# Optimization experiments

Measured on AMD Instinct MI355X. Metric: run time of the kernel, lower is better.

## Reference

```python
import jax, jax.numpy as jnp
import numpy as np

B, N, E, T, DIN, H, G, ND, NT, L = 4, 10000, 320000, 16, 16, 64, 64, 16, 3, 7


def _mlp2(x, W1, b1, W2, b2):
    # Linear -> LeakyReLU -> (Dropout: eval identity) -> Linear -> LeakyReLU
    h = jax.nn.leaky_relu(x @ W1 + b1)
    return jax.nn.leaky_relu(h @ W2 + b2)


def _gcn_conv(x, src, dst, ew, nt, W1, b1, W2, b2):
    # x: [B,N,D], nt: [B,N,ND], ew: [*,E,1] broadcastable over batch
    x_in = _mlp2(jnp.concatenate([x, nt], axis=-1), W1, b1, W2, b2)  # [B,N,G]
    msgs = x_in[:, src, :] * ew                                      # gather + weight, [B,E,G]
    aggr = jnp.zeros(x_in.shape, x_in.dtype).at[:, dst, :].add(msgs) # scatter-add, [B,N,G]
    return x + aggr


def _gru(x, Wx, Wh, bx, bh):
    # PyTorch-style GRU over time axis. x: [B,N,T,DIN] -> hs: [T,B,N,H]
    xw = jnp.einsum('bntd,dh->tbnh', x, Wx) + bx  # precompute input projections [T,B,N,3H]
    h0 = jnp.zeros(x.shape[:2] + (Wh.shape[0],), x.dtype)

    def step(h, xw_t):
        hw = h @ Wh + bh
        xr, xz, xn = jnp.split(xw_t, 3, axis=-1)
        hr, hz, hn = jnp.split(hw, 3, axis=-1)
        r = jax.nn.sigmoid(xr + hr)
        z = jax.nn.sigmoid(xz + hz)
        n = jnp.tanh(xn + r * hn)
        h_new = (1 - z) * n + z * h
        return h_new, h_new

    _, hs = jax.lax.scan(step, h0, xw)
    return hs


def reference(input_day, edge_attr, gru_Wx, gru_Wh, gru_bx, gru_bh,
              rnn_fc_W, rnn_fc_b,
              e_emb, e_c0_W1, e_c0_b1, e_c0_W2, e_c0_b2,
              e_c1_W1, e_c1_b1, e_c1_W2, e_c1_b2,
              e_fm_W1, e_fm_b1, e_fm_W2, e_fm_b2,
              g_emb, g_c0_W1, g_c0_b1, g_c0_W2, g_c0_b2,
              g_c1_W1, g_c1_b1, g_c1_W2, g_c1_b2,
              gcn_fc_W, gcn_fc_b,
              edge_index, node_type_ids):
    src, dst = edge_index[0], edge_index[1]

    # KRNN encoder (GRU) + max over time + FC head
    hs = _gru(input_day, gru_Wx, gru_Wh, gru_bx, gru_bh)  # [T,B,N,H]
    rnn_out = hs.max(axis=0)                              # kr_out.max(dim=-2) -> [B,N,H]
    y_rnn = rnn_out @ rnn_fc_W + rnn_fc_b                 # [B,N,L]

    # EdgeNet: GCN stack on static edge_attr, then per-edge pair MLP -> gate
    nt_e = jnp.broadcast_to(e_emb[node_type_ids][None], (B, N, ND))
    ew0 = edge_attr.reshape(1, E, 1)
    x = rnn_out
    x = _gcn_conv(x, src, dst, ew0, nt_e, e_c0_W1, e_c0_b1, e_c0_W2, e_c0_b2)
    x = _gcn_conv(x, src, dst, ew0, nt_e, e_c1_W1, e_c1_b1, e_c1_W2, e_c1_b2)
    edge_x = jnp.concatenate([x[:, src, :], x[:, dst, :]], axis=-1)  # [B,E,2G]
    h = jax.nn.leaky_relu(edge_x @ e_fm_W1 + e_fm_b1)
    edge_gate = jax.nn.relu(h @ e_fm_W2 + e_fm_b2)                   # [B,E,1]

    # Main GCNNet with learned edge gates
    nt_g = jnp.broadcast_to(g_emb[node_type_ids][None], (B, N, ND))
    x = rnn_out
    x = _gcn_conv(x, src, dst, edge_gate, nt_g, g_c0_W1, g_c0_b1, g_c0_W2, g_c0_b2)
    x = _gcn_conv(x, src, dst, edge_gate, nt_g, g_c1_W1, g_c1_b1, g_c1_W2, g_c1_b2)
    y_gcn = x @ gcn_fc_W + gcn_fc_b                                  # [B,N,L]

    return y_rnn + y_gcn


def setup_inputs() -> dict:
    key = jax.random.key(0)
    ks = iter(jax.random.split(key, 48))

    def nrm(shape, s=0.1):
        return jax.random.normal(next(ks), shape, jnp.float32) * s

    inp = {}
    inp['input_day'] = jax.random.normal(next(ks), (B, N, T, DIN), jnp.float32)
    inp['edge_index'] = jax.random.randint(next(ks), (2, E), 0, N)
    inp['node_type_ids'] = jax.random.randint(next(ks), (N,), 0, NT)
    inp['edge_attr'] = jax.random.uniform(next(ks), (E,), jnp.float32)

    inp['gru_Wx'] = nrm((DIN, 3 * H))
    inp['gru_Wh'] = nrm((H, 3 * H))
    inp['gru_bx'] = jnp.zeros((3 * H,), jnp.float32)
    inp['gru_bh'] = jnp.zeros((3 * H,), jnp.float32)
    inp['rnn_fc_W'] = nrm((H, L))
    inp['rnn_fc_b'] = jnp.zeros((L,), jnp.float32)

    inp['e_emb'] = nrm((NT, ND))
    inp['g_emb'] = nrm((NT, ND))
    for pre, in_dim in (('e_c0', H + ND), ('e_c1', G + ND), ('g_c0', H + ND), ('g_c1', G + ND)):
        inp[pre + '_W1'] = nrm((in_dim, G))
        inp[pre + '_b1'] = jnp.zeros((G,), jnp.float32)
        inp[pre + '_W2'] = nrm((G, G))
        inp[pre + '_b2'] = jnp.zeros((G,), jnp.float32)

    inp['e_fm_W1'] = nrm((2 * G, G))
    inp['e_fm_b1'] = jnp.zeros((G,), jnp.float32)
    inp['e_fm_W2'] = nrm((G, 1))
    inp['e_fm_b2'] = jnp.zeros((1,), jnp.float32)

    inp['gcn_fc_W'] = nrm((G, L))
    inp['gcn_fc_b'] = jnp.zeros((L,), jnp.float32)
    return inp
```

## Files before the change

### kernel.cpp

```cpp
#include <hip/hip_runtime.h>
#include <hip/hip_bf16.h>

#define NB 4
#define NN 10000
#define NE 320000
#define BN 40000
#define NL 7

typedef float f32x4 __attribute__((ext_vector_type(4)));
typedef __bf16 bf16x8 __attribute__((ext_vector_type(8)));

__device__ __forceinline__ float bf2f(unsigned short u){
  unsigned x = ((unsigned)u) << 16;
  return __builtin_bit_cast(float, x);
}
__device__ __forceinline__ unsigned short f2bf(float f){
  unsigned u = __builtin_bit_cast(unsigned, f);
  u += 0x7fffu + ((u >> 16) & 1u);
  return (unsigned short)(u >> 16);
}
__device__ __forceinline__ __bf16 f2b(float f){
  return __builtin_bit_cast(__bf16, f2bf(f));
}
__device__ __forceinline__ bf16x8 zero8(){
  uint4 z = make_uint4(0u,0u,0u,0u);
  return __builtin_bit_cast(bf16x8, z);
}
__device__ __forceinline__ bf16x8 one8(){
  uint4 z = make_uint4(0x3f80u,0u,0u,0u);
  return __builtin_bit_cast(bf16x8, z);
}
__device__ __forceinline__ bf16x8 ld8bf(const unsigned short* p){
  uint4 u = *(const uint4*)p;
  return __builtin_bit_cast(bf16x8, u);
}
__device__ __forceinline__ unsigned pk2(float lo, float hi){
  unsigned r;
  asm("v_cvt_pk_bf16_f32 %0, %1, %2" : "=v"(r) : "v"(lo), "v"(hi));
  return r;
}
__device__ __forceinline__ bf16x8 ld8f(const float* p){
  float4 a = *(const float4*)p;
  float4 b = *(const float4*)(p+4);
  uint4 u = make_uint4(pk2(a.x,a.y), pk2(a.z,a.w), pk2(b.x,b.y), pk2(b.z,b.w));
  return __builtin_bit_cast(bf16x8, u);
}
__device__ __forceinline__ float frcp(float x){ return __builtin_amdgcn_rcpf(x); }
__device__ __forceinline__ float sigm(float x){ return frcp(1.f+__expf(-x)); }
__device__ __forceinline__ float tanh_(float x){ return 1.f - 2.f*frcp(__expf(2.f*x)+1.f); }
__device__ __forceinline__ float lrelu(float x){ return x > 0.f ? x : 0.01f*x; }

#define LDS_WAIT() asm volatile("s_waitcnt lgkmcnt(0)" ::: "memory")

__global__ __launch_bounds__(256, 2) void gru_kernel(
    const float* __restrict__ xd,
    const float* __restrict__ Wx,
    const float* __restrict__ Wh,
    const float* __restrict__ bx,
    const float* __restrict__ bh,
    float* __restrict__ rnn)
{
  __shared__ __attribute__((aligned(16))) unsigned short WhT[192][72];
  __shared__ __attribute__((aligned(16))) unsigned short WxT[192][40];
  __shared__ __attribute__((aligned(16))) unsigned short hb[4][16][76];
  int tid = threadIdx.x;
  int wave = tid >> 6, lane = tid & 63;
  int ln16 = lane & 15, quad = lane >> 4;

  for (int i = tid; i < 64*192; i += 256){
    int k = i / 192, n = i - k*192;
    WhT[n][k] = f2bf(Wh[i]);
  }
  for (int i = tid; i < 16*192; i += 256){
    int k = i / 192, n = i - k*192;
    WxT[n][k] = f2bf(Wx[i]);
    WxT[n][17+k] = 0;
  }
  if (tid < 192){
    float bias = (tid < 128) ? (bx[tid] + bh[tid]) : bx[tid];
    WxT[tid][16] = f2bf(bias);
  }
  for (int i = tid; i < 4*16*76; i += 256) ((unsigned short*)hb)[i] = 0;
  __syncthreads();

  int rowbase = blockIdx.x * 64 + wave * 16;

  bf16x8 whf[2][12];
  #pragma unroll
  for (int kt=0; kt<2; ++kt)
    #pragma unroll
    for (int nt=0; nt<12; ++nt)
      whf[kt][nt] = ld8bf(&WhT[nt*16 + ln16][kt*32 + quad*8]);

  f32x4 bhn2[4];
  #pragma unroll
  for (int j=0;j<4;++j)
    bhn2[j] = *(const f32x4*)(bh + 128 + j*16 + quad*4);

  f32x4 hprev[4], vmax[4];
  #pragma unroll
  for (int j=0;j<4;++j){
    hprev[j] = (f32x4){0.f,0.f,0.f,0.f};
    vmax[j]  = (f32x4){-1e30f,-1e30f,-1e30f,-1e30f};
  }

  const float* xrow = xd + (size_t)(rowbase + ln16) * 256;
  unsigned short* hrow = &hb[wave][ln16][0];

  bf16x8 axc;
  if (quad < 2) axc = ld8f(xrow + quad*8);
  else          axc = (quad == 2) ? one8() : zero8();

  for (int t = 0; t < 16; ++t){
    bf16x8 axn;
    if (quad < 2) axn = (t < 15) ? ld8f(xrow + (t+1)*16 + quad*8) : zero8();
    else          axn = (quad == 2) ? one8() : zero8();
    bf16x8 ah0 = ld8bf(hrow + quad*8);
    bf16x8 ah1 = ld8bf(hrow + 32 + quad*8);

    #pragma unroll
    for (int j=0;j<4;++j){
      bf16x8 xr = ld8bf(&WxT[j*16+ln16][quad*8]);
      bf16x8 xz = ld8bf(&WxT[(4+j)*16+ln16][quad*8]);
      bf16x8 xn = ld8bf(&WxT[(8+j)*16+ln16][quad*8]);
      f32x4 z4 = (f32x4){0.f,0.f,0.f,0.f};
      f32x4 ar = __builtin_amdgcn_mfma_f32_16x16x32_bf16(xr, axc, z4, 0,0,0);
      ar = __builtin_amdgcn_mfma_f32_16x16x32_bf16(whf[0][j], ah0, ar, 0,0,0);
      ar = __builtin_amdgcn_mfma_f32_16x16x32_bf16(whf[1][j], ah1, ar, 0,0,0);
      f32x4 az = __builtin_amdgcn_mfma_f32_16x16x32_bf16(xz, axc, z4, 0,0,0);
      az = __builtin_amdgcn_mfma_f32_16x16x32_bf16(whf[0][4+j], ah0, az, 0,0,0);
      az = __builtin_amdgcn_mfma_f32_16x16x32_bf16(whf[1][4+j], ah1, az, 0,0,0);
      f32x4 an = __builtin_amdgcn_mfma_f32_16x16x32_bf16(xn, axc, z4, 0,0,0);
      f32x4 ah = __builtin_amdgcn_mfma_f32_16x16x32_bf16(whf[0][8+j], ah0, bhn2[j], 0,0,0);
      ah = __builtin_amdgcn_mfma_f32_16x16x32_bf16(whf[1][8+j], ah1, ah, 0,0,0);
      f32x4 hv;
      #pragma unroll
      for (int i=0;i<4;++i){
        float Er = __expf(-ar[i]);
        float Ez = __expf(-az[i]);
        float pr = 1.f + Er, pz = 1.f + Ez;
        float D  = frcp(pr * pz);
        float r  = D * pz;
        float z  = D * pr;
        float nn = tanh_(an[i] + r * ah[i]);
        float h  = fmaf(z, hprev[j][i]-nn, nn);
        hprev[j][i] = h;
        vmax[j][i] = fmaxf(vmax[j][i], h);
        hv[i] = h;
      }
      *(uint2*)&hb[wave][ln16][j*16+quad*4] = make_uint2(pk2(hv[0],hv[1]), pk2(hv[2],hv[3]));
    }
    LDS_WAIT();
    axc = axn;
  }
  float* orow = rnn + (size_t)(rowbase + ln16)*64;
  #pragma unroll
  for (int j=0;j<4;++j)
    *(f32x4*)(orow + j*16 + quad*4) = vmax[j];
}

__global__ __launch_bounds__(256, 2) void mlp2_kernel(
    const float* __restrict__ x,
    const int* __restrict__ ntid,
    const float* __restrict__ emb,
    const float* __restrict__ W1,
    const float* __restrict__ b1,
    const float* __restrict__ W2,
    const float* __restrict__ b2,
    unsigned short* __restrict__ out)
{
  __shared__ __attribute__((aligned(16))) unsigned short W1T[64][96];
  __shared__ __attribute__((aligned(16))) unsigned short W2T[64][72];
  __shared__ __attribute__((aligned(16))) unsigned short hb[4][16][72];
  __shared__ float sb1[64], sb2[64];
  int tid = threadIdx.x;
  for (int i=tid;i<80*64;i+=256){ int k=i>>6, n=i&63; W1T[n][k]=f2bf(W1[i]); }
  for (int i=tid;i<64*16;i+=256){ int n=i>>4, k=80+(i&15); W1T[n][k]=0; }
  for (int i=tid;i<64*64;i+=256){ int k=i>>6, n=i&63; W2T[n][k]=f2bf(W2[i]); }
  if (tid<64){ sb1[tid]=b1[tid]; sb2[tid]=b2[tid]; }
  __syncthreads();

  int wave = tid>>6, lane = tid&63, ln16 = lane&15, quad = lane>>4;
  int row0 = blockIdx.x*64 + wave*16;
  int r_ = row0 + ln16;
  const float* xr = x + (size_t)r_*64;
  bf16x8 a0 = ld8f(xr + quad*8);
  bf16x8 a1 = ld8f(xr + 32 + quad*8);
  int id = ntid[r_ % NN];
  bf16x8 a2 = (quad<2) ? ld8f(emb + id*16 + quad*8) : zero8();

  f32x4 acc[4];
  #pragma unroll
  for (int nt=0;nt<4;++nt){
    float bb = sb1[nt*16+ln16];
    acc[nt] = (f32x4){bb,bb,bb,bb};
    acc[nt] = __builtin_amdgcn_mfma_f32_16x16x32_bf16(a0, ld8bf(&W1T[nt*16+ln16][quad*8]),    acc[nt], 0,0,0);
    acc[nt] = __builtin_amdgcn_mfma_f32_16x16x32_bf16(a1, ld8bf(&W1T[nt*16+ln16][32+quad*8]), acc[nt], 0,0,0);
    acc[nt] = __builtin_amdgcn_mfma_f32_16x16x32_bf16(a2, ld8bf(&W1T[nt*16+ln16][64+quad*8]), acc[nt], 0,0,0);
  }
  #pragma unroll
  for (int nt=0;nt<4;++nt)
    #pragma unroll
    for (int i=0;i<4;++i)
      hb[wave][quad*4+i][nt*16+ln16] = f2bf(lrelu(acc[nt][i]));
  LDS_WAIT();
  bf16x8 h0 = ld8bf(&hb[wave][ln16][quad*8]);
  bf16x8 h1 = ld8bf(&hb[wave][ln16][32+quad*8]);
  f32x4 acc2[4];
  #pragma unroll
  for (int nt=0;nt<4;++nt){
    float bb = sb2[nt*16+ln16];
    acc2[nt] = (f32x4){bb,bb,bb,bb};
    acc2[nt] = __builtin_amdgcn_mfma_f32_16x16x32_bf16(h0, ld8bf(&W2T[nt*16+ln16][quad*8]),    acc2[nt], 0,0,0);
    acc2[nt] = __builtin_amdgcn_mfma_f32_16x16x32_bf16(h1, ld8bf(&W2T[nt*16+ln16][32+quad*8]), acc2[nt], 0,0,0);
  }
  #pragma unroll
  for (int nt=0;nt<4;++nt)
    #pragma unroll
    for (int i=0;i<4;++i)
      out[(size_t)(row0+quad*4+i)*64 + nt*16+ln16] = f2bf(lrelu(acc2[nt][i]));
}

__global__ __launch_bounds__(256, 2) void uv_kernel(
    const float* __restrict__ x,
    const float* __restrict__ W1,
    unsigned short* __restrict__ uvp)
{
  __shared__ __attribute__((aligned(16))) unsigned short WT[128][72];
  int tid=threadIdx.x;
  for (int i=tid;i<64*64;i+=256){
    int k=i>>6, n=i&63;
    WT[n][k]    = f2bf(W1[i]);
    WT[64+n][k] = f2bf(W1[64*64 + i]);
  }
  __syncthreads();
  int wave=tid>>6, lane=tid&63, ln16=lane&15, quad=lane>>4;
  int row0 = blockIdx.x*64 + wave*16;
  const float* xr = x + (size_t)(row0+ln16)*64;
  bf16x8 a0 = ld8f(xr + quad*8);
  bf16x8 a1 = ld8f(xr + 32 + quad*8);
  f32x4 acc[8];
  #pragma unroll
  for (int nt=0;nt<8;++nt){
    acc[nt] = (f32x4){0.f,0.f,0.f,0.f};
    acc[nt] = __builtin_amdgcn_mfma_f32_16x16x32_bf16(a0, ld8bf(&WT[nt*16+ln16][quad*8]),    acc[nt], 0,0,0);
    acc[nt] = __builtin_amdgcn_mfma_f32_16x16x32_bf16(a1, ld8bf(&WT[nt*16+ln16][32+quad*8]), acc[nt], 0,0,0);
  }
  #pragma unroll
  for (int nt=0;nt<8;++nt)
    #pragma unroll
    for (int i=0;i<4;++i)
      uvp[(size_t)(row0+quad*4+i)*128 + nt*16+ln16] = f2bf(acc[nt][i]);
}

__global__ __launch_bounds__(256) void count_kernel(const int* __restrict__ ei, int* __restrict__ counts){
  int e = blockIdx.x*256+threadIdx.x;
  atomicAdd(&counts[ei[NE+e]], 1);
}
__global__ __launch_bounds__(1024) void scan_kernel(const int* __restrict__ counts,
                                                    int* __restrict__ rowptr, int* __restrict__ cursor){
  __shared__ int incl[10240];
  __shared__ int wsum[16];
  int tid=threadIdx.x, wave=tid>>6, lane=tid&63;
  int base = wave*640;
  int carry=0;
  #pragma unroll
  for (int c=0;c<10;++c){
    int i = base + c*64 + lane;
    int v = (i<NN)? counts[i] : 0;
    int s = v;
    #pragma unroll
    for (int off=1;off<64;off<<=1){
      int t_ = __shfl_up(s, off);
      if (lane>=off) s += t_;
    }
    s += carry;
    incl[base + c*64 + lane] = s;
    carry = __shfl(s, 63);
  }
  if (lane==63) wsum[wave]=carry;
  __syncthreads();
  if (wave==0){
    int w_ = (lane<16)? wsum[lane]:0;
    #pragma unroll
    for (int off=1;off<16;off<<=1){
      int t_ = __shfl_up(w_, off);
      if (lane>=off) w_ += t_;
    }
    if (lane<16) wsum[lane]=w_;
  }
  __syncthreads();
  int woff = (wave>0)? wsum[wave-1] : 0;
  #pragma unroll
  for (int c=0;c<10;++c){
    int i = base + c*64 + lane;
    if (i<NN){
      int excl = incl[i] + woff - counts[i];
      rowptr[i]=excl; cursor[i]=excl;
    }
  }
  if (tid==0) rowptr[NN]=wsum[15];
}
__global__ __launch_bounds__(256) void fill_kernel(const int* __restrict__ ei,
                                                   const float* __restrict__ ea,
                                                   int* __restrict__ cursor,
                                                   int* __restrict__ ssrc,
                                                   float* __restrict__ wcsr){
  int e = blockIdx.x*256+threadIdx.x;
  int d = ei[NE+e];
  int pos = atomicAdd(&cursor[d],1);
  ssrc[pos]=ei[e];
  wcsr[pos]=ea[e];
}

__global__ __launch_bounds__(256) void aggr_kernel(
    const float* x,
    const unsigned short* __restrict__ xin,
    const int* __restrict__ rowptr,
    const int* __restrict__ ssrc,
    const float* __restrict__ wp,
    int bstride,
    float* out)
{
  int tid=threadIdx.x;
  int wave=tid>>6, lane=tid&63;
  int sub=lane>>4, l=lane&15;
  int bid = blockIdx.x*4 + wave;
  int b = bid / NN, n = bid - b*NN;
  int p0 = rowptr[n], p1 = rowptr[n+1];
  const unsigned short* xb_ = xin + (size_t)b*NN*64;
  const float* wb = wp + (size_t)b*bstride;
  float a0=0.f, a1=0.f, a2=0.f, a3=0.f;
  #pragma unroll 4
  for (int p=p0+sub; p<p1; p+=4){
    int s = ssrc[p];
    float w = wb[p];
    uint2 m = *(const uint2*)(xb_ + (size_t)s*64 + l*4);
    a0 += bf2f((unsigned short)(m.x & 0xffffu)) * w;
    a1 += bf2f((unsigned short)(m.x >> 16)) * w;
    a2 += bf2f((unsigned short)(m.y & 0xffffu)) * w;
    a3 += bf2f((unsigned short)(m.y >> 16)) * w;
  }
  a0 += __shfl_xor(a0,16); a0 += __shfl_xor(a0,32);
  a1 += __shfl_xor(a1,16); a1 += __shfl_xor(a1,32);
  a2 += __shfl_xor(a2,16); a2 += __shfl_xor(a2,32);
  a3 += __shfl_xor(a3,16); a3 += __shfl_xor(a3,32);
  if (sub==0){
    float4 base = *(const float4*)(x + (size_t)bid*64 + l*4);
    float4 o; o.x=base.x+a0; o.y=base.y+a1; o.z=base.z+a2; o.w=base.w+a3;
    *(float4*)(out + (size_t)bid*64 + l*4) = o;
  }
}

__global__ __launch_bounds__(256) void aggr_final_kernel(
    const float* x,
    const unsigned short* __restrict__ xin,
    const int* __restrict__ rowptr,
    const int* __restrict__ ssrc,
    const float* __restrict__ wp,
    const float* __restrict__ rnn,
    const float* __restrict__ Wr, const float* __restrict__ br,
    const float* __restrict__ Wg, const float* __restrict__ bg,
    float* __restrict__ out)
{
  __shared__ float sWr[448], sWg[448], sb[7];
  int tid=threadIdx.x;
  for (int i=tid;i<448;i+=256){ sWr[i]=Wr[i]; sWg[i]=Wg[i]; }
  if (tid<7) sb[tid]=br[tid]+bg[tid];
  __syncthreads();
  int wave=tid>>6, lane=tid&63;
  int sub=lane>>4, l=lane&15;
  int bid = blockIdx.x*4 + wave;
  int b = bid / NN, n = bid - b*NN;
  int p0 = rowptr[n], p1 = rowptr[n+1];
  const unsigned short* xb_ = xin + (size_t)b*NN*64;
  const float* wb = wp + (size_t)b*NE;
  float a0=0.f, a1=0.f, a2=0.f, a3=0.f;
  #pragma unroll 4
  for (int p=p0+sub; p<p1; p+=4){
    int s = ssrc[p];
    float w = wb[p];
    uint2 m = *(const uint2*)(xb_ + (size_t)s*64 + l*4);
    a0 += bf2f((unsigned short)(m.x & 0xffffu)) * w;
    a1 += bf2f((unsigned short)(m.x >> 16)) * w;
    a2 += bf2f((unsigned short)(m.y & 0xffffu)) * w;
    a3 += bf2f((unsigned short)(m.y >> 16)) * w;
  }
  a0 += __shfl_xor(a0,16); a0 += __shfl_xor(a0,32);
  a1 += __shfl_xor(a1,16); a1 += __shfl_xor(a1,32);
  a2 += __shfl_xor(a2,16); a2 += __shfl_xor(a2,32);
  a3 += __shfl_xor(a3,16); a3 += __shfl_xor(a3,32);
  if (sub==0){
    float4 base = *(const float4*)(x + (size_t)bid*64 + l*4);
    float o0=base.x+a0, o1=base.y+a1, o2=base.z+a2, o3=base.w+a3;
    float4 rr = *(const float4*)(rnn + (size_t)bid*64 + l*4);
    float part[7];
    #pragma unroll
    for (int q=0;q<7;++q)
      part[q] = o0*sWg[(l*4+0)*7+q] + o1*sWg[(l*4+1)*7+q]
              + o2*sWg[(l*4+2)*7+q] + o3*sWg[(l*4+3)*7+q]
              + rr.x*sWr[(l*4+0)*7+q] + rr.y*sWr[(l*4+1)*7+q]
              + rr.z*sWr[(l*4+2)*7+q] + rr.w*sWr[(l*4+3)*7+q];
    #pragma unroll
    for (int q=0;q<7;++q){
      part[q] += __shfl_xor(part[q],1);
      part[q] += __shfl_xor(part[q],2);
      part[q] += __shfl_xor(part[q],4);
      part[q] += __shfl_xor(part[q],8);
    }
    if (l==0){
      #pragma unroll
      for (int q=0;q<7;++q) out[(size_t)bid*7+q] = part[q] + sb[q];
    }
  }
}

__global__ __launch_bounds__(256) void gate_kernel(
    const unsigned short* __restrict__ uvp,
    const int* __restrict__ rowptr,
    const int* __restrict__ ssrc,
    const float* __restrict__ b1,
    const float* __restrict__ W2,
    const float* __restrict__ b2,
    float* __restrict__ gate)
{
  int tid=threadIdx.x;
  int wave=tid>>6, lane=tid&63;
  int sub=lane>>4, l=lane&15;
  int bid = blockIdx.x*4 + wave;
  int b = bid / NN, n = bid - b*NN;
  int p0 = rowptr[n], p1 = rowptr[n+1];
  const unsigned short* ub = uvp + (size_t)b*NN*128;
  uint2 vu = *(const uint2*)(ub + (size_t)n*128 + 64 + l*4);
  float v0=bf2f((unsigned short)(vu.x&0xffffu)), v1=bf2f((unsigned short)(vu.x>>16));
  float v2=bf2f((unsigned short)(vu.y&0xffffu)), v3=bf2f((unsigned short)(vu.y>>16));
  float4 bb = *(const float4*)(b1 + l*4);
  float4 ww = *(const float4*)(W2 + l*4);
  float b2v = b2[0];
  float* gb = gate + (size_t)b*NE;
  #pragma unroll 4
  for (int p=p0+sub; p<p1; p+=4){
    int s = ssrc[p];
    uint2 uu = *(const uint2*)(ub + (size_t)s*128 + l*4);
    float h0 = lrelu(bf2f((unsigned short)(uu.x&0xffffu)) + v0 + bb.x);
    float h1 = lrelu(bf2f((unsigned short)(uu.x>>16))     + v1 + bb.y);
    float h2 = lrelu(bf2f((unsigned short)(uu.y&0xffffu)) + v2 + bb.z);
    float h3 = lrelu(bf2f((unsigned short)(uu.y>>16))     + v3 + bb.w);
    float part = h0*ww.x + h1*ww.y + h2*ww.z + h3*ww.w;
    part += __shfl_xor(part,1);
    part += __shfl_xor(part,2);
    part += __shfl_xor(part,4);
    part += __shfl_xor(part,8);
    if (l==0){
      float g = part + b2v;
      gb[p] = g>0.f ? g : 0.f;
    }
  }
}

extern "C" void kernel_launch(void* const* d_in, const int* in_sizes, int n_in,
                              void* d_out, int out_size, void* d_ws, size_t ws_size,
                              hipStream_t stream)
{
  (void)in_sizes; (void)n_in; (void)out_size; (void)ws_size;
  const float* input_day = (const float*)d_in[0];
  const int* ei    = (const int*)d_in[1];
  const int* ntid  = (const int*)d_in[2];
  const float* edge_attr = (const float*)d_in[3];
  const float* gWx = (const float*)d_in[4];
  const float* gWh = (const float*)d_in[5];
  const float* gbx = (const float*)d_in[6];
  const float* gbh = (const float*)d_in[7];
  const float* rW  = (const float*)d_in[8];
  const float* rb  = (const float*)d_in[9];
  const float* eemb= (const float*)d_in[10];
  const float* gemb= (const float*)d_in[11];
  const float* ec0W1=(const float*)d_in[12];
  const float* ec0b1=(const float*)d_in[13];
  const float* ec0W2=(const float*)d_in[14];
  const float* ec0b2=(const float*)d_in[15];
  const float* ec1W1=(const float*)d_in[16];
  const float* ec1b1=(const float*)d_in[17];
  const float* ec1W2=(const float*)d_in[18];
  const float* ec1b2=(const float*)d_in[19];
  const float* gc0W1=(const float*)d_in[20];
  const float* gc0b1=(const float*)d_in[21];
  const float* gc0W2=(const float*)d_in[22];
  const float* gc0b2=(const float*)d_in[23];
  const float* gc1W1=(const float*)d_in[24];
  const float* gc1b1=(const float*)d_in[25];
  const float* gc1W2=(const float*)d_in[26];
  const float* gc1b2=(const float*)d_in[27];
  const float* efmW1=(const float*)d_in[28];
  const float* efmb1=(const float*)d_in[29];
  const float* efmW2=(const float*)d_in[30];
  const float* efmb2=(const float*)d_in[31];
  const float* gcnW =(const float*)d_in[32];
  const float* gcnb =(const float*)d_in[33];

  char* ws = (char*)d_ws;
  float*          rnn = (float*)(ws);
  float*          xe  = (float*)(ws + 10240000);
  unsigned short* xin = (unsigned short*)(ws + 20480000);
  unsigned short* uvp = (unsigned short*)(ws + 25600000);
  float*          gat = (float*)(ws + 35840000);
  int* rowptr= (int*)(ws + 40960000);
  int* cursor= (int*)(ws + 41000064);
  int* counts= (int*)(ws + 41040064);
  int*   ssrc= (int*)(ws + 41080064);
  float* wcsr= (float*)(ws + 42360064);

  hipMemsetAsync(counts, 0, NN*sizeof(int), stream);
  count_kernel<<<NE/256, 256, 0, stream>>>(ei, counts);
  scan_kernel<<<1, 1024, 0, stream>>>(counts, rowptr, cursor);
  fill_kernel<<<NE/256, 256, 0, stream>>>(ei, edge_attr, cursor, ssrc, wcsr);

  gru_kernel<<<625, 256, 0, stream>>>(input_day, gWx, gWh, gbx, gbh, rnn);

  mlp2_kernel<<<625, 256, 0, stream>>>(rnn, ntid, eemb, ec0W1, ec0b1, ec0W2, ec0b2, xin);
  aggr_kernel<<<BN/4, 256, 0, stream>>>(rnn, xin, rowptr, ssrc, wcsr, 0, xe);
  mlp2_kernel<<<625, 256, 0, stream>>>(xe, ntid, eemb, ec1W1, ec1b1, ec1W2, ec1b2, xin);
  aggr_kernel<<<BN/4, 256, 0, stream>>>(xe, xin, rowptr, ssrc, wcsr, 0, xe);

  uv_kernel<<<625, 256, 0, stream>>>(xe, efmW1, uvp);
  gate_kernel<<<BN/4, 256, 0, stream>>>(uvp, rowptr, ssrc, efmb1, efmW2, efmb2, gat);

  mlp2_kernel<<<625, 256, 0, stream>>>(rnn, ntid, gemb, gc0W1, gc0b1, gc0W2, gc0b2, xin);
  aggr_kernel<<<BN/4, 256, 0, stream>>>(rnn, xin, rowptr, ssrc, gat, NE, xe);
  mlp2_kernel<<<625, 256, 0, stream>>>(xe, ntid, gemb, gc1W1, gc1b1, gc1W2, gc1b2, xin);
  aggr_final_kernel<<<BN/4, 256, 0, stream>>>(xe, xin, rowptr, ssrc, gat, rnn,
                                              rW, rb, gcnW, gcnb, (float*)d_out);
}
```

Measured before the change: 462.2 us.

## Fuse GCN aggregation with following MLP and UV projection kernels

Merges each neighbour-aggregation pass with the next per-node MLP (or the UV projection) into one kernel handling 16 rows per block, so the aggregated features are handed over through LDS instead of being written to global memory and read back. Workspace buffers are reused as ping-pong inputs so a fused kernel never overwrites the buffer it is still gathering from. In exchange, each node's edges are now walked serially by 16 lanes rather than split over four sub-groups, every block reloads and converts the weight matrices, and the launch grid grows to 2500 blocks.

```diff
diff --git a/kernel.cpp b/kernel.cpp
--- a/kernel.cpp
+++ b/kernel.cpp
@@ -19,9 +19,6 @@
   u += 0x7fffu + ((u >> 16) & 1u);
   return (unsigned short)(u >> 16);
 }
-__device__ __forceinline__ __bf16 f2b(float f){
-  return __builtin_bit_cast(__bf16, f2bf(f));
-}
 __device__ __forceinline__ bf16x8 zero8(){
   uint4 z = make_uint4(0u,0u,0u,0u);
   return __builtin_bit_cast(bf16x8, z);
@@ -46,7 +43,6 @@
   return __builtin_bit_cast(bf16x8, u);
 }
 __device__ __forceinline__ float frcp(float x){ return __builtin_amdgcn_rcpf(x); }
-__device__ __forceinline__ float sigm(float x){ return frcp(1.f+__expf(-x)); }
 __device__ __forceinline__ float tanh_(float x){ return 1.f - 2.f*frcp(__expf(2.f*x)+1.f); }
 __device__ __forceinline__ float lrelu(float x){ return x > 0.f ? x : 0.01f*x; }
 
@@ -221,36 +217,142 @@
       out[(size_t)(row0+quad*4+i)*64 + nt*16+ln16] = f2bf(lrelu(acc2[nt][i]));
 }
 
-__global__ __launch_bounds__(256, 2) void uv_kernel(
+__global__ __launch_bounds__(256) void aggr_mlp_kernel(
     const float* __restrict__ x,
+    const unsigned short* __restrict__ xin,
+    const int* __restrict__ rowptr,
+    const int* __restrict__ ssrc,
+    const float* __restrict__ wp,
+    int bstride,
+    const int* __restrict__ ntid,
+    const float* __restrict__ emb,
+    const float* __restrict__ W1,
+    const float* __restrict__ b1,
+    const float* __restrict__ W2,
+    const float* __restrict__ b2,
+    float* __restrict__ xe_out,
+    unsigned short* __restrict__ out)
+{
+  __shared__ __attribute__((aligned(16))) unsigned short W1T[64][96];
+  __shared__ __attribute__((aligned(16))) unsigned short W2T[64][72];
+  __shared__ __attribute__((aligned(16))) unsigned short hb[16][72];
+  __shared__ __attribute__((aligned(16))) unsigned short h2[16][72];
+  __shared__ float sb1[64], sb2[64];
+  int tid = threadIdx.x;
+  for (int i=tid;i<80*64;i+=256){ int k=i>>6, n=i&63; W1T[n][k]=f2bf(W1[i]); }
+  for (int i=tid;i<64*16;i+=256){ int n=i>>4, k=80+(i&15); W1T[n][k]=0; }
+  for (int i=tid;i<64*64;i+=256){ int k=i>>6, n=i&63; W2T[n][k]=f2bf(W2[i]); }
+  if (tid<64){ sb1[tid]=b1[tid]; sb2[tid]=b2[tid]; }
+
+  int wave = tid>>6, lane = tid&63, ln16 = lane&15, quad = lane>>4;
+  int row0 = blockIdx.x*16;
+  int b = row0 / NN;
+  int r = wave*4 + quad;
+  int row = row0 + r;
+  int n = row - b*NN;
+  int l = ln16;
+  int p0 = rowptr[n], p1 = rowptr[n+1];
+  const unsigned short* xb_ = xin + (size_t)b*NN*64;
+  const float* wb = wp + (size_t)b*bstride;
+  float a0=0.f, a1=0.f, a2=0.f, a3=0.f;
+  #pragma unroll 4
+  for (int p=p0; p<p1; ++p){
+    int s = ssrc[p];
+    float w = wb[p];
+    uint2 m = *(const uint2*)(xb_ + (size_t)s*64 + l*4);
+    a0 += bf2f((unsigned short)(m.x & 0xffffu)) * w;
+    a1 += bf2f((unsigned short)(m.x >> 16)) * w;
+    a2 += bf2f((unsigned short)(m.y & 0xffffu)) * w;
+    a3 += bf2f((unsigned short)(m.y >> 16)) * w;
+  }
+  float4 base = *(const float4*)(x + (size_t)row*64 + l*4);
+  float o0=base.x+a0, o1=base.y+a1, o2=base.z+a2, o3=base.w+a3;
+  float4 ov; ov.x=o0; ov.y=o1; ov.z=o2; ov.w=o3;
+  *(float4*)(xe_out + (size_t)row*64 + l*4) = ov;
+  *(uint2*)&hb[r][l*4] = make_uint2(pk2(o0,o1), pk2(o2,o3));
+  __syncthreads();
+
+  int id = ntid[row0 + ln16 - b*NN];
+  bf16x8 xa0 = ld8bf(&hb[ln16][quad*8]);
+  bf16x8 xa1 = ld8bf(&hb[ln16][32+quad*8]);
+  bf16x8 xa2 = (quad<2) ? ld8f(emb + id*16 + quad*8) : zero8();
+  float bb = sb1[wave*16+ln16];
+  f32x4 acc = (f32x4){bb,bb,bb,bb};
+  acc = __builtin_amdgcn_mfma_f32_16x16x32_bf16(xa0, ld8bf(&W1T[wave*16+ln16][quad*8]),    acc, 0,0,0);
+  acc = __builtin_amdgcn_mfma_f32_16x16x32_bf16(xa1, ld8bf(&W1T[wave*16+ln16][32+quad*8]), acc, 0,0,0);
+  acc = __builtin_amdgcn_mfma_f32_16x16x32_bf16(xa2, ld8bf(&W1T[wave*16+ln16][64+quad*8]), acc, 0,0,0);
+  #pragma unroll
+  for (int i=0;i<4;++i)
+    h2[quad*4+i][wave*16+ln16] = f2bf(lrelu(acc[i]));
+  __syncthreads();
+  bf16x8 hh0 = ld8bf(&h2[ln16][quad*8]);
+  bf16x8 hh1 = ld8bf(&h2[ln16][32+quad*8]);
+  float b2v = sb2[wave*16+ln16];
+  f32x4 acc2 = (f32x4){b2v,b2v,b2v,b2v};
+  acc2 = __builtin_amdgcn_mfma_f32_16x16x32_bf16(hh0, ld8bf(&W2T[wave*16+ln16][quad*8]),    acc2, 0,0,0);
+  acc2 = __builtin_amdgcn_mfma_f32_16x16x32_bf16(hh1, ld8bf(&W2T[wave*16+ln16][32+quad*8]), acc2, 0,0,0);
+  #pragma unroll
+  for (int i=0;i<4;++i)
+    out[(size_t)(row0+quad*4+i)*64 + wave*16+ln16] = f2bf(lrelu(acc2[i]));
+}
+
+__global__ __launch_bounds__(256) void aggr_uv_kernel(
+    const float* __restrict__ x,
+    const unsigned short* __restrict__ xin,
+    const int* __restrict__ rowptr,
+    const int* __restrict__ ssrc,
+    const float* __restrict__ wp,
+    int bstride,
     const float* __restrict__ W1,
     unsigned short* __restrict__ uvp)
 {
   __shared__ __attribute__((aligned(16))) unsigned short WT[128][72];
-  int tid=threadIdx.x;
+  __shared__ __attribute__((aligned(16))) unsigned short hb[16][72];
+  int tid = threadIdx.x;
   for (int i=tid;i<64*64;i+=256){
     int k=i>>6, n=i&63;
     WT[n][k]    = f2bf(W1[i]);
     WT[64+n][k] = f2bf(W1[64*64 + i]);
   }
-  __syncthreads();
-  int wave=tid>>6, lane=tid&63, ln16=lane&15, quad=lane>>4;
-  int row0 = blockIdx.x*64 + wave*16;
-  const float* xr = x + (size_t)(row0+ln16)*64;
-  bf16x8 a0 = ld8f(xr + quad*8);
-  bf16x8 a1 = ld8f(xr + 32 + quad*8);
-  f32x4 acc[8];
-  #pragma unroll
-  for (int nt=0;nt<8;++nt){
-    acc[nt] = (f32x4){0.f,0.f,0.f,0.f};
-    acc[nt] = __builtin_amdgcn_mfma_f32_16x16x32_bf16(a0, ld8bf(&WT[nt*16+ln16][quad*8]),    acc[nt], 0,0,0);
-    acc[nt] = __builtin_amdgcn_mfma_f32_16x16x32_bf16(a1, ld8bf(&WT[nt*16+ln16][32+quad*8]), acc[nt], 0,0,0);
-  }
-  #pragma unroll
-  for (int nt=0;nt<8;++nt)
+
+  int wave = tid>>6, lane = tid&63, ln16 = lane&15, quad = lane>>4;
+  int row0 = blockIdx.x*16;
+  int b = row0 / NN;
+  int r = wave*4 + quad;
+  int row = row0 + r;
+  int n = row - b*NN;
+  int l = ln16;
+  int p0 = rowptr[n], p1 = rowptr[n+1];
+  const unsigned short* xb_ = xin + (size_t)b*NN*64;
+  const float* wb = wp + (size_t)b*bstride;
+  float a0=0.f, a1=0.f, a2=0.f, a3=0.f;
+  #pragma unroll 4
+  for (int p=p0; p<p1; ++p){
+    int s = ssrc[p];
+    float w = wb[p];
+    uint2 m = *(const uint2*)(xb_ + (size_t)s*64 + l*4);
+    a0 += bf2f((unsigned short)(m.x & 0xffffu)) * w;
+    a1 += bf2f((unsigned short)(m.x >> 16)) * w;
+    a2 += bf2f((unsigned short)(m.y & 0xffffu)) * w;
+    a3 += bf2f((unsigned short)(m.y >> 16)) * w;
+  }
+  float4 base = *(const float4*)(x + (size_t)row*64 + l*4);
+  float o0=base.x+a0, o1=base.y+a1, o2=base.z+a2, o3=base.w+a3;
+  *(uint2*)&hb[r][l*4] = make_uint2(pk2(o0,o1), pk2(o2,o3));
+  __syncthreads();
+
+  bf16x8 xa0 = ld8bf(&hb[ln16][quad*8]);
+  bf16x8 xa1 = ld8bf(&hb[ln16][32+quad*8]);
+  #pragma unroll
+  for (int t=0;t<2;++t){
+    int nt = wave*2 + t;
+    f32x4 acc = (f32x4){0.f,0.f,0.f,0.f};
+    acc = __builtin_amdgcn_mfma_f32_16x16x32_bf16(xa0, ld8bf(&WT[nt*16+ln16][quad*8]),    acc, 0,0,0);
+    acc = __builtin_amdgcn_mfma_f32_16x16x32_bf16(xa1, ld8bf(&WT[nt*16+ln16][32+quad*8]), acc, 0,0,0);
     #pragma unroll
     for (int i=0;i<4;++i)
-      uvp[(size_t)(row0+quad*4+i)*128 + nt*16+ln16] = f2bf(acc[nt][i]);
+      uvp[(size_t)(row0+quad*4+i)*128 + nt*16+ln16] = f2bf(acc[i]);
+  }
 }
 
 __global__ __launch_bounds__(256) void count_kernel(const int* __restrict__ ei, int* __restrict__ counts){
@@ -311,45 +413,6 @@
   int pos = atomicAdd(&cursor[d],1);
   ssrc[pos]=ei[e];
   wcsr[pos]=ea[e];
-}
-
-__global__ __launch_bounds__(256) void aggr_kernel(
-    const float* x,
-    const unsigned short* __restrict__ xin,
-    const int* __restrict__ rowptr,
-    const int* __restrict__ ssrc,
-    const float* __restrict__ wp,
-    int bstride,
-    float* out)
-{
-  int tid=threadIdx.x;
-  int wave=tid>>6, lane=tid&63;
-  int sub=lane>>4, l=lane&15;
-  int bid = blockIdx.x*4 + wave;
-  int b = bid / NN, n = bid - b*NN;
-  int p0 = rowptr[n], p1 = rowptr[n+1];
-  const unsigned short* xb_ = xin + (size_t)b*NN*64;
-  const float* wb = wp + (size_t)b*bstride;
-  float a0=0.f, a1=0.f, a2=0.f, a3=0.f;
-  #pragma unroll 4
-  for (int p=p0+sub; p<p1; p+=4){
-    int s = ssrc[p];
-    float w = wb[p];
-    uint2 m = *(const uint2*)(xb_ + (size_t)s*64 + l*4);
-    a0 += bf2f((unsigned short)(m.x & 0xffffu)) * w;
-    a1 += bf2f((unsigned short)(m.x >> 16)) * w;
-    a2 += bf2f((unsigned short)(m.y & 0xffffu)) * w;
-    a3 += bf2f((unsigned short)(m.y >> 16)) * w;
-  }
-  a0 += __shfl_xor(a0,16); a0 += __shfl_xor(a0,32);
-  a1 += __shfl_xor(a1,16); a1 += __shfl_xor(a1,32);
-  a2 += __shfl_xor(a2,16); a2 += __shfl_xor(a2,32);
-  a3 += __shfl_xor(a3,16); a3 += __shfl_xor(a3,32);
-  if (sub==0){
-    float4 base = *(const float4*)(x + (size_t)bid*64 + l*4);
-    float4 o; o.x=base.x+a0; o.y=base.y+a1; o.z=base.z+a2; o.w=base.w+a3;
-    *(float4*)(out + (size_t)bid*64 + l*4) = o;
-  }
 }
 
 __global__ __launch_bounds__(256) void aggr_final_kernel(
@@ -501,7 +564,7 @@
   char* ws = (char*)d_ws;
   float*          rnn = (float*)(ws);
   float*          xe  = (float*)(ws + 10240000);
-  unsigned short* xin = (unsigned short*)(ws + 20480000);
+  unsigned short* xinA= (unsigned short*)(ws + 20480000);
   unsigned short* uvp = (unsigned short*)(ws + 25600000);
   float*          gat = (float*)(ws + 35840000);
   int* rowptr= (int*)(ws + 40960000);
@@ -509,6 +572,8 @@
   int* counts= (int*)(ws + 41040064);
   int*   ssrc= (int*)(ws + 41080064);
   float* wcsr= (float*)(ws + 42360064);
+  unsigned short* xinB = (unsigned short*)gat;
+  unsigned short* xinD = (unsigned short*)uvp;
 
   hipMemsetAsync(counts, 0, NN*sizeof(int), stream);
   count_kernel<<<NE/256, 256, 0, stream>>>(ei, counts);
@@ -517,17 +582,18 @@
 
   gru_kernel<<<625, 256, 0, stream>>>(input_day, gWx, gWh, gbx, gbh, rnn);
 
-  mlp2_kernel<<<625, 256, 0, stream>>>(rnn, ntid, eemb, ec0W1, ec0b1, ec0W2, ec0b2, xin);
-  aggr_kernel<<<BN/4, 256, 0, stream>>>(rnn, xin, rowptr, ssrc, wcsr, 0, xe);
-  mlp2_kernel<<<625, 256, 0, stream>>>(xe, ntid, eemb, ec1W1, ec1b1, ec1W2, ec1b2, xin);
-  aggr_kernel<<<BN/4, 256, 0, stream>>>(xe, xin, rowptr, ssrc, wcsr, 0, xe);
-
-  uv_kernel<<<625, 256, 0, stream>>>(xe, efmW1, uvp);
+  mlp2_kernel<<<625, 256, 0, stream>>>(rnn, ntid, eemb, ec0W1, ec0b1, ec0W2, ec0b2, xinA);
+  aggr_mlp_kernel<<<BN/16, 256, 0, stream>>>(rnn, xinA, rowptr, ssrc, wcsr, 0,
+                                             ntid, eemb, ec1W1, ec1b1, ec1W2, ec1b2,
+                                             xe, xinB);
+  aggr_uv_kernel<<<BN/16, 256, 0, stream>>>(xe, xinB, rowptr, ssrc, wcsr, 0,
+                                            efmW1, uvp);
   gate_kernel<<<BN/4, 256, 0, stream>>>(uvp, rowptr, ssrc, efmb1, efmW2, efmb2, gat);
 
-  mlp2_kernel<<<625, 256, 0, stream>>>(rnn, ntid, gemb, gc0W1, gc0b1, gc0W2, gc0b2, xin);
-  aggr_kernel<<<BN/4, 256, 0, stream>>>(rnn, xin, rowptr, ssrc, gat, NE, xe);
-  mlp2_kernel<<<625, 256, 0, stream>>>(xe, ntid, gemb, gc1W1, gc1b1, gc1W2, gc1b2, xin);
-  aggr_final_kernel<<<BN/4, 256, 0, stream>>>(xe, xin, rowptr, ssrc, gat, rnn,
+  mlp2_kernel<<<625, 256, 0, stream>>>(rnn, ntid, gemb, gc0W1, gc0b1, gc0W2, gc0b2, xinA);
+  aggr_mlp_kernel<<<BN/16, 256, 0, stream>>>(rnn, xinA, rowptr, ssrc, gat, NE,
+                                             ntid, gemb, gc1W1, gc1b1, gc1W2, gc1b2,
+                                             xe, xinD);
+  aggr_final_kernel<<<BN/4, 256, 0, stream>>>(xe, xinD, rowptr, ssrc, gat, rnn,
                                               rW, rb, gcnW, gcnb, (float*)d_out);
 }
```

New measurement: 461.1 us. About the same (-0.2%).
